# Kernel tuning notes

Measured on AMD Instinct MI355X. Metric: run time of the kernel, lower is better.

## Reference

```python
import jax, jax.numpy as jnp
import numpy as np

N, E, D, A = 50000, 800000, 128, 5


def _glorot(key, shape):
    fan = shape[0] + shape[1]
    s = jnp.sqrt(6.0 / fan)
    return jax.random.uniform(key, shape, jnp.float32, -s, s)


def setup_inputs() -> dict:
    key = jax.random.key(0)
    ks = jax.random.split(key, 16)
    x = jax.random.normal(ks[0], (N, D), jnp.float32)
    edge_index = jax.random.randint(ks[1], (2, E), 0, N, jnp.int32)
    return {
        "x": x,
        "anchor_node": _glorot(ks[2], (A, D)),          # NodePromptplus.anchor_prompt
        "attn_w": _glorot(ks[3], (D, A)),               # NodePromptplus.attention (in,out)
        "attn_b": jnp.zeros((A,), jnp.float32),
        "anchor_edge": _glorot(ks[4], (A, D)),          # EdgePromptplus.anchor_prompt
        "w_w": _glorot(ks[5], (2 * D, A)),              # EdgePromptplus.w[0]
        "w_b": jnp.zeros((A,), jnp.float32),
        "cd1_w": _glorot(ks[6], (2 * D, D)),            # causal_discovery Linear1
        "cd1_b": jnp.zeros((D,), jnp.float32),
        "cd2_w": _glorot(ks[7], (D, D)),                # causal_discovery Linear2
        "cd2_b": jnp.zeros((D,), jnp.float32),
        "int_w": _glorot(ks[8], (D, D)),                # intervention Linear
        "int_b": jnp.zeros((D,), jnp.float32),
        "edge_index": edge_index,
        "layer": 0,
    }


def reference(x, anchor_node, attn_w, attn_b, anchor_edge, w_w, w_b,
              cd1_w, cd1_b, cd2_w, cd2_b, int_w, int_b, edge_index, layer):
    # --- NodePromptplus.add ---
    w = jax.nn.softmax(x @ attn_w + attn_b, axis=1)            # [N,A]
    node_px = x + w @ anchor_node                              # [N,D]
    # --- EdgePromptplus.get_prompt ---
    src, dst = edge_index[0], edge_index[1]
    combined_x = jnp.concatenate([x[src], x[dst]], axis=1)     # [E,2D]
    b = jax.nn.softmax(jax.nn.leaky_relu(combined_x @ w_w + w_b), axis=1)  # [E,A]
    edge_prompt = b @ anchor_edge                              # [E,D]
    # --- index_add scatter to both endpoints ---
    agg = jnp.zeros_like(x).at[src].add(edge_prompt).at[dst].add(edge_prompt)
    # --- causal discovery gating + intervention ---
    combined = jnp.concatenate([node_px, agg], axis=1)         # [N,2D]
    h = jax.nn.relu(combined @ cd1_w + cd1_b)
    causal_strength = jax.nn.sigmoid(h @ cd2_w + cd2_b)        # [N,D]
    intervened = (node_px + agg) @ int_w + int_b               # [N,D]
    final_x = node_px + causal_strength * intervened
    return final_x, edge_prompt
```

## Files before the change

kernel.cpp:

```cpp
#include <hip/hip_runtime.h>
#include <math.h>

#define D 128
#define A 5
#define TM 64
#define CSTR 68

__global__ __launch_bounds__(256) void node_prompt_kernel(
    const float* __restrict__ x,
    const float* __restrict__ attn_w, const float* __restrict__ attn_b,
    const float* __restrict__ anchor_node,
    float* __restrict__ node_px, int N)
{
    int t = threadIdx.x;
    int j = (t & 63) * 2;
    float At0[A], At1[A], AN0[A], AN1[A], Ab[A];
    #pragma unroll
    for (int a = 0; a < A; a++) {
        At0[a] = attn_w[(size_t)j * A + a];
        At1[a] = attn_w[(size_t)(j + 1) * A + a];
        AN0[a] = anchor_node[a * D + j];
        AN1[a] = anchor_node[a * D + j + 1];
        Ab[a]  = attn_b[a];
    }
    int wid = blockIdx.x * 4 + (t >> 6);
    int nw  = gridDim.x * 4;
    for (int n = wid; n < N; n += nw) {
        float2 xv = *(const float2*)&x[(size_t)n * D + j];
        float l[A];
        #pragma unroll
        for (int a = 0; a < A; a++) {
            float p = xv.x * At0[a] + xv.y * At1[a];
            #pragma unroll
            for (int off = 32; off; off >>= 1) p += __shfl_xor(p, off);
            l[a] = p + Ab[a];
        }
        float m = l[0];
        #pragma unroll
        for (int a = 1; a < A; a++) m = fmaxf(m, l[a]);
        float s = 0.f;
        #pragma unroll
        for (int a = 0; a < A; a++) { l[a] = __expf(l[a] - m); s += l[a]; }
        float inv = 1.f / s;
        float2 o = xv;
        #pragma unroll
        for (int a = 0; a < A; a++) {
            float w = l[a] * inv;
            o.x += w * AN0[a];
            o.y += w * AN1[a];
        }
        *(float2*)&node_px[(size_t)n * D + j] = o;
    }
}

__global__ __launch_bounds__(256) void edge_kernel(
    const float* __restrict__ x, const int* __restrict__ ei,
    const float* __restrict__ w_w, const float* __restrict__ w_b,
    const float* __restrict__ anchor_edge,
    float* __restrict__ edge_prompt, float* __restrict__ bagg, int E, int N)
{
    int t = threadIdx.x;
    int j = (t & 63) * 2;
    float W0[A], W1[A], W2[A], W3[A], AE0[A], AE1[A], Wb[A];
    #pragma unroll
    for (int a = 0; a < A; a++) {
        W0[a]  = w_w[(size_t)j * A + a];
        W1[a]  = w_w[(size_t)(j + 1) * A + a];
        W2[a]  = w_w[(size_t)(D + j) * A + a];
        W3[a]  = w_w[(size_t)(D + j + 1) * A + a];
        AE0[a] = anchor_edge[a * D + j];
        AE1[a] = anchor_edge[a * D + j + 1];
        Wb[a]  = w_b[a];
    }
    int sub = t & 31;
    int half = (t & 63) >> 5;

    int wid = blockIdx.x * 4 + (t >> 6);
    int nw  = gridDim.x * 4;
    for (int e = wid; e < E; e += nw) {
        int s = ei[e];
        int d = ei[(size_t)E + e];
        float2 xs = *(const float2*)&x[(size_t)s * D + j];
        float2 xd = *(const float2*)&x[(size_t)d * D + j];
        float l[A];
        #pragma unroll
        for (int a = 0; a < A; a++) {
            float p = xs.x * W0[a] + xs.y * W1[a]
                    + xd.x * W2[a] + xd.y * W3[a];
            #pragma unroll
            for (int off = 32; off; off >>= 1) p += __shfl_xor(p, off);
            p += Wb[a];
            l[a] = (p > 0.f) ? p : 0.01f * p;
        }
        float m = l[0];
        #pragma unroll
        for (int a = 1; a < A; a++) m = fmaxf(m, l[a]);
        float sum = 0.f;
        #pragma unroll
        for (int a = 0; a < A; a++) { l[a] = __expf(l[a] - m); sum += l[a]; }
        float inv = 1.f / sum;
        float2 ep = make_float2(0.f, 0.f);
        #pragma unroll
        for (int a = 0; a < A; a++) {
            float b = l[a] * inv;
            ep.x += b * AE0[a];
            ep.y += b * AE1[a];
        }
        *(float2*)&edge_prompt[(size_t)e * D + j] = ep;

        if (sub < A) {
            float bv = 0.f;
            #pragma unroll
            for (int a = 0; a < A; a++) if (sub == a) bv = l[a] * inv;
            int node = half ? d : s;
            atomicAdd(&bagg[(size_t)node * A + sub], bv);
        }
    }
}

__global__ __launch_bounds__(256) void agg_kernel(
    const float* __restrict__ bagg, const float* __restrict__ anchor_edge,
    float* __restrict__ agg, int N)
{
    __shared__ float AE[A * D];
    int t = threadIdx.x;
    for (int f = t; f < A * D; f += 256) AE[f] = anchor_edge[f];
    __syncthreads();
    int total = N * (D / 4);
    for (int i = blockIdx.x * 256 + t; i < total; i += gridDim.x * 256) {
        int n = i >> 5;
        int c = (i & 31) * 4;
        const float* br = &bagg[(size_t)n * A];
        float b0 = br[0], b1 = br[1], b2 = br[2], b3 = br[3], b4 = br[4];
        float4 e0 = *(float4*)&AE[0 * D + c];
        float4 e1 = *(float4*)&AE[1 * D + c];
        float4 e2 = *(float4*)&AE[2 * D + c];
        float4 e3 = *(float4*)&AE[3 * D + c];
        float4 e4 = *(float4*)&AE[4 * D + c];
        float4 r;
        r.x = b0 * e0.x + b1 * e1.x + b2 * e2.x + b3 * e3.x + b4 * e4.x;
        r.y = b0 * e0.y + b1 * e1.y + b2 * e2.y + b3 * e3.y + b4 * e4.y;
        r.z = b0 * e0.z + b1 * e1.z + b2 * e2.z + b3 * e3.z + b4 * e4.z;
        r.w = b0 * e0.w + b1 * e1.w + b2 * e2.w + b3 * e3.w + b4 * e4.w;
        *(float4*)&agg[(size_t)n * D + c] = r;
    }
}

__device__ __forceinline__ void fma4(float4& acc, const float4 cv,
                                     const float4 w0, const float4 w1,
                                     const float4 w2, const float4 w3)
{
    acc.x += cv.x * w0.x + cv.y * w1.x + cv.z * w2.x + cv.w * w3.x;
    acc.y += cv.x * w0.y + cv.y * w1.y + cv.z * w2.y + cv.w * w3.y;
    acc.z += cv.x * w0.z + cv.y * w1.z + cv.z * w2.z + cv.w * w3.z;
    acc.w += cv.x * w0.w + cv.y * w1.w + cv.z * w2.w + cv.w * w3.w;
}

__global__ __launch_bounds__(256) void cd1_kernel(
    const float* __restrict__ node_px, const float* __restrict__ agg,
    const float* __restrict__ cd1_w, const float* __restrict__ cd1_b,
    float* __restrict__ h, int N)
{
    __shared__ float Wt[64 * D];
    __shared__ float Cn[TM * CSTR];
    int t = threadIdx.x;
    int n0 = blockIdx.x * TM;
    int cg = t & 31, ng = t >> 5;
    int c0 = cg * 4;
    float4 acc[8];
    #pragma unroll
    for (int jj = 0; jj < 8; jj++) acc[jj] = make_float4(0.f, 0.f, 0.f, 0.f);

    for (int kt = 0; kt < 4; kt++) {
        int k0 = kt * 64;
        __syncthreads();
        const float4* Wg = (const float4*)(cd1_w + (size_t)k0 * D);
        float4* Wl = (float4*)Wt;
        #pragma unroll
        for (int i = 0; i < 8; i++) Wl[i * 256 + t] = Wg[i * 256 + t];
        const float* src = (k0 < 128) ? node_px : agg;
        int koff = k0 & 127;
        #pragma unroll
        for (int i = 0; i < 4; i++) {
            int f = i * 256 + t;
            int n = f >> 4, k4 = f & 15;
            int nn = n0 + n; if (nn >= N) nn = N - 1;
            float4 v = *(const float4*)&src[(size_t)nn * D + koff + k4 * 4];
            *(float4*)&Cn[n * CSTR + k4 * 4] = v;
        }
        __syncthreads();
        #pragma unroll 4
        for (int k4 = 0; k4 < 16; k4++) {
            float4 w0 = *(float4*)&Wt[(k4 * 4 + 0) * D + c0];
            float4 w1 = *(float4*)&Wt[(k4 * 4 + 1) * D + c0];
            float4 w2 = *(float4*)&Wt[(k4 * 4 + 2) * D + c0];
            float4 w3 = *(float4*)&Wt[(k4 * 4 + 3) * D + c0];
            #pragma unroll
            for (int jj = 0; jj < 8; jj++) {
                float4 cv = *(float4*)&Cn[(ng * 8 + jj) * CSTR + k4 * 4];
                fma4(acc[jj], cv, w0, w1, w2, w3);
            }
        }
    }
    float4 b = *(const float4*)&cd1_b[c0];
    #pragma unroll
    for (int jj = 0; jj < 8; jj++) {
        int n = n0 + ng * 8 + jj;
        if (n < N) {
            float4 r;
            r.x = fmaxf(acc[jj].x + b.x, 0.f);
            r.y = fmaxf(acc[jj].y + b.y, 0.f);
            r.z = fmaxf(acc[jj].z + b.z, 0.f);
            r.w = fmaxf(acc[jj].w + b.w, 0.f);
            *(float4*)&h[(size_t)n * D + c0] = r;
        }
    }
}

__global__ __launch_bounds__(256) void cd2_kernel(
    const float* h_in, const float* __restrict__ cd2_w,
    const float* __restrict__ cd2_b, float* cs_out, int N)
{
    __shared__ float Wt[64 * D];
    __shared__ float Cn[TM * CSTR];
    int t = threadIdx.x;
    int n0 = blockIdx.x * TM;
    int cg = t & 31, ng = t >> 5;
    int c0 = cg * 4;
    float4 acc[8];
    #pragma unroll
    for (int jj = 0; jj < 8; jj++) acc[jj] = make_float4(0.f, 0.f, 0.f, 0.f);

    for (int kt = 0; kt < 2; kt++) {
        int k0 = kt * 64;
        __syncthreads();
        const float4* Wg = (const float4*)(cd2_w + (size_t)k0 * D);
        float4* Wl = (float4*)Wt;
        #pragma unroll
        for (int i = 0; i < 8; i++) Wl[i * 256 + t] = Wg[i * 256 + t];
        #pragma unroll
        for (int i = 0; i < 4; i++) {
            int f = i * 256 + t;
            int n = f >> 4, k4 = f & 15;
            int nn = n0 + n; if (nn >= N) nn = N - 1;
            float4 v = *(const float4*)&h_in[(size_t)nn * D + k0 + k4 * 4];
            *(float4*)&Cn[n * CSTR + k4 * 4] = v;
        }
        __syncthreads();
        #pragma unroll 4
        for (int k4 = 0; k4 < 16; k4++) {
            float4 w0 = *(float4*)&Wt[(k4 * 4 + 0) * D + c0];
            float4 w1 = *(float4*)&Wt[(k4 * 4 + 1) * D + c0];
            float4 w2 = *(float4*)&Wt[(k4 * 4 + 2) * D + c0];
            float4 w3 = *(float4*)&Wt[(k4 * 4 + 3) * D + c0];
            #pragma unroll
            for (int jj = 0; jj < 8; jj++) {
                float4 cv = *(float4*)&Cn[(ng * 8 + jj) * CSTR + k4 * 4];
                fma4(acc[jj], cv, w0, w1, w2, w3);
            }
        }
    }
    float4 b = *(const float4*)&cd2_b[c0];
    #pragma unroll
    for (int jj = 0; jj < 8; jj++) {
        int n = n0 + ng * 8 + jj;
        if (n < N) {
            float4 r;
            r.x = 1.f / (1.f + __expf(-(acc[jj].x + b.x)));
            r.y = 1.f / (1.f + __expf(-(acc[jj].y + b.y)));
            r.z = 1.f / (1.f + __expf(-(acc[jj].z + b.z)));
            r.w = 1.f / (1.f + __expf(-(acc[jj].w + b.w)));
            *(float4*)&cs_out[(size_t)n * D + c0] = r;
        }
    }
}

__global__ __launch_bounds__(256) void final_kernel(
    const float* node_px, const float* __restrict__ agg,
    const float* __restrict__ cs, const float* __restrict__ int_w,
    const float* __restrict__ int_b, float* final_x, int N)
{
    __shared__ float Wt[64 * D];
    __shared__ float Cn[TM * CSTR];
    int t = threadIdx.x;
    int n0 = blockIdx.x * TM;
    int cg = t & 31, ng = t >> 5;
    int c0 = cg * 4;
    float4 acc[8];
    #pragma unroll
    for (int jj = 0; jj < 8; jj++) acc[jj] = make_float4(0.f, 0.f, 0.f, 0.f);

    for (int kt = 0; kt < 2; kt++) {
        int k0 = kt * 64;
        __syncthreads();
        const float4* Wg = (const float4*)(int_w + (size_t)k0 * D);
        float4* Wl = (float4*)Wt;
        #pragma unroll
        for (int i = 0; i < 8; i++) Wl[i * 256 + t] = Wg[i * 256 + t];
        #pragma unroll
        for (int i = 0; i < 4; i++) {
            int f = i * 256 + t;
            int n = f >> 4, k4 = f & 15;
            int nn = n0 + n; if (nn >= N) nn = N - 1;
            float4 a4 = *(const float4*)&node_px[(size_t)nn * D + k0 + k4 * 4];
            float4 b4 = *(const float4*)&agg[(size_t)nn * D + k0 + k4 * 4];
            float4 v = make_float4(a4.x + b4.x, a4.y + b4.y, a4.z + b4.z, a4.w + b4.w);
            *(float4*)&Cn[n * CSTR + k4 * 4] = v;
        }
        __syncthreads();
        #pragma unroll 4
        for (int k4 = 0; k4 < 16; k4++) {
            float4 w0 = *(float4*)&Wt[(k4 * 4 + 0) * D + c0];
            float4 w1 = *(float4*)&Wt[(k4 * 4 + 1) * D + c0];
            float4 w2 = *(float4*)&Wt[(k4 * 4 + 2) * D + c0];
            float4 w3 = *(float4*)&Wt[(k4 * 4 + 3) * D + c0];
            #pragma unroll
            for (int jj = 0; jj < 8; jj++) {
                float4 cv = *(float4*)&Cn[(ng * 8 + jj) * CSTR + k4 * 4];
                fma4(acc[jj], cv, w0, w1, w2, w3);
            }
        }
    }
    float4 b = *(const float4*)&int_b[c0];
    #pragma unroll
    for (int jj = 0; jj < 8; jj++) {
        int n = n0 + ng * 8 + jj;
        if (n < N) {
            float4 iv = make_float4(acc[jj].x + b.x, acc[jj].y + b.y,
                                    acc[jj].z + b.z, acc[jj].w + b.w);
            float4 c4 = *(const float4*)&cs[(size_t)n * D + c0];
            float4 np = *(const float4*)&node_px[(size_t)n * D + c0];
            float4 r;
            r.x = np.x + c4.x * iv.x;
            r.y = np.y + c4.y * iv.y;
            r.z = np.z + c4.z * iv.z;
            r.w = np.w + c4.w * iv.w;
            *(float4*)&final_x[(size_t)n * D + c0] = r;
        }
    }
}

extern "C" void kernel_launch(void* const* d_in, const int* in_sizes, int n_in,
                              void* d_out, int out_size, void* d_ws, size_t ws_size,
                              hipStream_t stream)
{
    const float* x           = (const float*)d_in[0];
    const float* anchor_node = (const float*)d_in[1];
    const float* attn_w      = (const float*)d_in[2];
    const float* attn_b      = (const float*)d_in[3];
    const float* anchor_edge = (const float*)d_in[4];
    const float* w_w         = (const float*)d_in[5];
    const float* w_b         = (const float*)d_in[6];
    const float* cd1_w       = (const float*)d_in[7];
    const float* cd1_b       = (const float*)d_in[8];
    const float* cd2_w       = (const float*)d_in[9];
    const float* cd2_b       = (const float*)d_in[10];
    const float* int_w       = (const float*)d_in[11];
    const float* int_b       = (const float*)d_in[12];
    const int*   ei          = (const int*)d_in[13];

    int N = in_sizes[0] / D;
    int E = in_sizes[13] / 2;

    float* out         = (float*)d_out;
    float* node_px     = out;
    float* edge_prompt = out + (size_t)N * D;
    float* agg         = (float*)d_ws;
    float* h           = agg + (size_t)N * D;
    float* bagg        = h;

    hipMemsetAsync(bagg, 0, (size_t)N * A * sizeof(float), stream);

    node_prompt_kernel<<<512, 256, 0, stream>>>(x, attn_w, attn_b, anchor_node, node_px, N);
    edge_kernel<<<2048, 256, 0, stream>>>(x, ei, w_w, w_b, anchor_edge, edge_prompt, bagg, E, N);
    agg_kernel<<<2048, 256, 0, stream>>>(bagg, anchor_edge, agg, N);

    int nb = (N + TM - 1) / TM;
    cd1_kernel<<<nb, 256, 0, stream>>>(node_px, agg, cd1_w, cd1_b, h, N);
    cd2_kernel<<<nb, 256, 0, stream>>>(h, cd2_w, cd2_b, h, N);
    final_kernel<<<nb, 256, 0, stream>>>(node_px, agg, h, int_w, int_b, node_px, N);
}
```

Baseline: 889.1 us.

## Precompute per-node edge logits to avoid gathering full feature rows per edge

The edge attention logits are linear in x[src] and x[dst], so the per-node projections x@W_top and x@W_bottom are now computed once per node inside the node prompt kernel and stored as small [N,5] arrays. The edge kernel then gathers only 5 floats per endpoint instead of two 128-wide rows, and uses one thread per edge for the softmax and atomics. The edge prompt rows are written as coalesced float4 stores after staging the softmax weights in shared memory. This removes about 800K×2×512 bytes of random gathers, in exchange for extra reductions in the node kernel and workspace for the two logit arrays.

```diff
diff --git a/kernel.cpp b/kernel.cpp
--- a/kernel.cpp
+++ b/kernel.cpp
@@ -10,11 +10,15 @@
     const float* __restrict__ x,
     const float* __restrict__ attn_w, const float* __restrict__ attn_b,
     const float* __restrict__ anchor_node,
-    float* __restrict__ node_px, int N)
-{
-    int t = threadIdx.x;
-    int j = (t & 63) * 2;
+    const float* __restrict__ w_w,
+    float* __restrict__ node_px,
+    float* __restrict__ lsrc, float* __restrict__ ldst, int N)
+{
+    int t = threadIdx.x;
+    int lane = t & 63;
+    int j = lane * 2;
     float At0[A], At1[A], AN0[A], AN1[A], Ab[A];
+    float W0[A], W1[A], W2[A], W3[A];
     #pragma unroll
     for (int a = 0; a < A; a++) {
         At0[a] = attn_w[(size_t)j * A + a];
@@ -22,18 +26,30 @@
         AN0[a] = anchor_node[a * D + j];
         AN1[a] = anchor_node[a * D + j + 1];
         Ab[a]  = attn_b[a];
+        W0[a]  = w_w[(size_t)j * A + a];
+        W1[a]  = w_w[(size_t)(j + 1) * A + a];
+        W2[a]  = w_w[(size_t)(D + j) * A + a];
+        W3[a]  = w_w[(size_t)(D + j + 1) * A + a];
     }
     int wid = blockIdx.x * 4 + (t >> 6);
     int nw  = gridDim.x * 4;
     for (int n = wid; n < N; n += nw) {
         float2 xv = *(const float2*)&x[(size_t)n * D + j];
-        float l[A];
+        float l[A], es[A], ed[A];
         #pragma unroll
         for (int a = 0; a < A; a++) {
-            float p = xv.x * At0[a] + xv.y * At1[a];
+            float p0 = xv.x * At0[a] + xv.y * At1[a];
+            float p1 = xv.x * W0[a]  + xv.y * W1[a];
+            float p2 = xv.x * W2[a]  + xv.y * W3[a];
             #pragma unroll
-            for (int off = 32; off; off >>= 1) p += __shfl_xor(p, off);
-            l[a] = p + Ab[a];
+            for (int off = 32; off; off >>= 1) {
+                p0 += __shfl_xor(p0, off);
+                p1 += __shfl_xor(p1, off);
+                p2 += __shfl_xor(p2, off);
+            }
+            l[a]  = p0 + Ab[a];
+            es[a] = p1;
+            ed[a] = p2;
         }
         float m = l[0];
         #pragma unroll
@@ -50,46 +66,43 @@
             o.y += w * AN1[a];
         }
         *(float2*)&node_px[(size_t)n * D + j] = o;
+        if (lane < A) {
+            float vs = es[0], vd = ed[0];
+            #pragma unroll
+            for (int a = 1; a < A; a++) if (lane == a) { vs = es[a]; vd = ed[a]; }
+            lsrc[(size_t)n * A + lane] = vs;
+            ldst[(size_t)n * A + lane] = vd;
+        }
     }
 }
 
 __global__ __launch_bounds__(256) void edge_kernel(
-    const float* __restrict__ x, const int* __restrict__ ei,
-    const float* __restrict__ w_w, const float* __restrict__ w_b,
-    const float* __restrict__ anchor_edge,
-    float* __restrict__ edge_prompt, float* __restrict__ bagg, int E, int N)
-{
-    int t = threadIdx.x;
-    int j = (t & 63) * 2;
-    float W0[A], W1[A], W2[A], W3[A], AE0[A], AE1[A], Wb[A];
-    #pragma unroll
-    for (int a = 0; a < A; a++) {
-        W0[a]  = w_w[(size_t)j * A + a];
-        W1[a]  = w_w[(size_t)(j + 1) * A + a];
-        W2[a]  = w_w[(size_t)(D + j) * A + a];
-        W3[a]  = w_w[(size_t)(D + j + 1) * A + a];
-        AE0[a] = anchor_edge[a * D + j];
-        AE1[a] = anchor_edge[a * D + j + 1];
-        Wb[a]  = w_b[a];
-    }
-    int sub = t & 31;
-    int half = (t & 63) >> 5;
-
-    int wid = blockIdx.x * 4 + (t >> 6);
-    int nw  = gridDim.x * 4;
-    for (int e = wid; e < E; e += nw) {
+    const int* __restrict__ ei,
+    const float* __restrict__ lsrc, const float* __restrict__ ldst,
+    const float* __restrict__ w_b, const float* __restrict__ anchor_edge,
+    float* __restrict__ edge_prompt, float* __restrict__ bagg, int E)
+{
+    __shared__ float Bs[256 * A];
+    int t = threadIdx.x;
+    int cg = t & 31;
+    float4 AEc[A];
+    #pragma unroll
+    for (int a = 0; a < A; a++) AEc[a] = *(const float4*)&anchor_edge[a * D + cg * 4];
+    float Wb[A];
+    #pragma unroll
+    for (int a = 0; a < A; a++) Wb[a] = w_b[a];
+
+    int base = blockIdx.x * 256;
+    int e = base + t;
+    if (e < E) {
         int s = ei[e];
         int d = ei[(size_t)E + e];
-        float2 xs = *(const float2*)&x[(size_t)s * D + j];
-        float2 xd = *(const float2*)&x[(size_t)d * D + j];
+        const float* ps = &lsrc[(size_t)s * A];
+        const float* pd = &ldst[(size_t)d * A];
         float l[A];
         #pragma unroll
         for (int a = 0; a < A; a++) {
-            float p = xs.x * W0[a] + xs.y * W1[a]
-                    + xd.x * W2[a] + xd.y * W3[a];
-            #pragma unroll
-            for (int off = 32; off; off >>= 1) p += __shfl_xor(p, off);
-            p += Wb[a];
+            float p = ps[a] + pd[a] + Wb[a];
             l[a] = (p > 0.f) ? p : 0.01f * p;
         }
         float m = l[0];
@@ -99,22 +112,32 @@
         #pragma unroll
         for (int a = 0; a < A; a++) { l[a] = __expf(l[a] - m); sum += l[a]; }
         float inv = 1.f / sum;
-        float2 ep = make_float2(0.f, 0.f);
         #pragma unroll
         for (int a = 0; a < A; a++) {
-            float b = l[a] * inv;
-            ep.x += b * AE0[a];
-            ep.y += b * AE1[a];
-        }
-        *(float2*)&edge_prompt[(size_t)e * D + j] = ep;
-
-        if (sub < A) {
-            float bv = 0.f;
-            #pragma unroll
-            for (int a = 0; a < A; a++) if (sub == a) bv = l[a] * inv;
-            int node = half ? d : s;
-            atomicAdd(&bagg[(size_t)node * A + sub], bv);
-        }
+            float bv = l[a] * inv;
+            Bs[t * A + a] = bv;
+            atomicAdd(&bagg[(size_t)s * A + a], bv);
+            atomicAdd(&bagg[(size_t)d * A + a], bv);
+        }
+    }
+    __syncthreads();
+    int eg = t >> 5;
+    #pragma unroll 4
+    for (int r = 0; r < 32; r++) {
+        int row = eg * 32 + r;
+        int e2 = base + row;
+        if (e2 >= E) break;
+        float b0 = Bs[row * A + 0];
+        float b1 = Bs[row * A + 1];
+        float b2 = Bs[row * A + 2];
+        float b3 = Bs[row * A + 3];
+        float b4 = Bs[row * A + 4];
+        float4 rr;
+        rr.x = b0 * AEc[0].x + b1 * AEc[1].x + b2 * AEc[2].x + b3 * AEc[3].x + b4 * AEc[4].x;
+        rr.y = b0 * AEc[0].y + b1 * AEc[1].y + b2 * AEc[2].y + b3 * AEc[3].y + b4 * AEc[4].y;
+        rr.z = b0 * AEc[0].z + b1 * AEc[1].z + b2 * AEc[2].z + b3 * AEc[3].z + b4 * AEc[4].z;
+        rr.w = b0 * AEc[0].w + b1 * AEc[1].w + b2 * AEc[2].w + b3 * AEc[3].w + b4 * AEc[4].w;
+        *(float4*)&edge_prompt[(size_t)e2 * D + cg * 4] = rr;
     }
 }
 
@@ -368,11 +391,16 @@
     float* agg         = (float*)d_ws;
     float* h           = agg + (size_t)N * D;
     float* bagg        = h;
+    float* lsrc        = h + (size_t)N * A;
+    float* ldst        = h + (size_t)2 * N * A;
 
     hipMemsetAsync(bagg, 0, (size_t)N * A * sizeof(float), stream);
 
-    node_prompt_kernel<<<512, 256, 0, stream>>>(x, attn_w, attn_b, anchor_node, node_px, N);
-    edge_kernel<<<2048, 256, 0, stream>>>(x, ei, w_w, w_b, anchor_edge, edge_prompt, bagg, E, N);
+    node_prompt_kernel<<<512, 256, 0, stream>>>(x, attn_w, attn_b, anchor_node, w_w,
+                                                node_px, lsrc, ldst, N);
+    int nb_e = (E + 255) / 256;
+    edge_kernel<<<nb_e, 256, 0, stream>>>(ei, lsrc, ldst, w_b, anchor_edge,
+                                          edge_prompt, bagg, E);
     agg_kernel<<<2048, 256, 0, stream>>>(bagg, anchor_edge, agg, N);
 
     int nb = (N + TM - 1) / TM;
```

New measurement: 1.016 ms. +14.3%, slower.
